# Optimization experiments

Measured on AMD Instinct MI355X. Metric: run time of the kernel, lower is better.

The kernel has to match this reference:

```python
import jax, jax.numpy as jnp
import numpy as np

WB = 8   # weight bit width (signed int8, power-of-two scale)
AB = 8   # activation bit width (uint8, power-of-two scale)
BB = 8   # bias bit width

# (name, c_in, c_out, kernel) for every QuantConv2d in order
_CFG = [("1", 3, 32, 3), ("2", 32, 16, 3), ("31", 16, 16, 1), ("32", 16, 32, 3),
        ("33", 32, 32, 1), ("34", 32, 64, 3), ("41", 64, 32, 1), ("42", 32, 64, 3),
        ("43", 64, 32, 1), ("44", 32, 64, 3), ("45", 64, 32, 1), ("46", 32, 64, 3)]
_POOL_AFTER = {"1", "2", "34"}  # MaxPool2d(2,2) follows these blocks


def _ste_round(x):
    # straight-through rounding (Brevitas-style fake quant)
    return x + jax.lax.stop_gradient(jnp.round(x) - x)


def _p2_scale(maxv, levels):
    # power-of-two (fixed point) per-tensor scale covering maxv with `levels` steps
    maxv = jnp.maximum(jax.lax.stop_gradient(maxv), 1e-8)
    return 2.0 ** jnp.ceil(jnp.log2(maxv / levels))


def quant_int(x, bw):
    # signed symmetric fixed-point fake quant (Int8WeightPerTensorFixedPoint style)
    n = 2.0 ** (bw - 1) - 1.0
    s = _p2_scale(jnp.max(jnp.abs(x)), n)
    return jnp.clip(_ste_round(x / s), -n - 1.0, n) * s


def quant_uint(x, bw):
    # unsigned fixed-point fake quant (Uint8ActPerTensorFixedPoint style)
    n = 2.0 ** bw - 1.0
    s = _p2_scale(jnp.max(x), n)
    return jnp.clip(_ste_round(x / s), 0.0, n) * s


def _conv(x, w, pad):
    return jax.lax.conv_general_dilated(
        x, w, window_strides=(1, 1), padding=[(pad, pad), (pad, pad)],
        dimension_numbers=("NCHW", "OIHW", "NCHW"))


def _maxpool2(x):
    return jax.lax.reduce_window(x, -jnp.inf, jax.lax.max,
                                 (1, 1, 2, 2), (1, 1, 2, 2), "VALID")


def _forward(x, p):
    # QuantIdentity on input (uint8 fixed point)
    x = quant_uint(x, AB)
    for n, ci, co, k in _CFG:
        pad = (k - 1) // 2
        y = _conv(x, quant_int(p["w" + n], WB), pad)               # quantized conv, no bias
        # BatchNorm2dToQuantScaleBias: per-channel affine with quantized scale/bias
        y = (y * quant_int(p["sg" + n], WB)[None, :, None, None]
             + quant_int(p["sb" + n], BB)[None, :, None, None])
        x = quant_uint(jax.nn.relu(y), AB)                          # QuantReLU
        if n in _POOL_AFTER:
            x = _maxpool2(x)
    # TruncAvgPool2d(28,28) over the remaining 28x28 map + RoundTo8bit requant
    x = quant_uint(jnp.mean(x, axis=(2, 3)), 8)                     # [B, 64]
    h = x @ quant_int(p["fw1"], WB).T + quant_int(p["fb1"], BB)     # linear51
    h = quant_uint(jax.nn.relu(h), AB)                              # relu5
    return h @ quant_int(p["fw2"], WB).T + quant_int(p["fb2"], BB)  # linear52


def setup_inputs() -> dict:
    key = jax.random.key(0)
    ks = iter(jax.random.split(key, 64))
    inp = {"x": jax.random.uniform(next(ks), (16, 3, 224, 224), jnp.float32)}
    for n, ci, co, k in _CFG:
        inp["w" + n] = jax.random.normal(next(ks), (co, ci, k, k), jnp.float32) * 0.1
        inp["sg" + n] = jax.random.uniform(next(ks), (co,), jnp.float32, 0.5, 1.5)
        inp["sb" + n] = jax.random.normal(next(ks), (co,), jnp.float32) * 0.1
    inp["fw1"] = jax.random.normal(next(ks), (16, 64), jnp.float32) * 0.1
    inp["fb1"] = jax.random.normal(next(ks), (16,), jnp.float32) * 0.1
    inp["fw2"] = jax.random.normal(next(ks), (10, 16), jnp.float32) * 0.1
    inp["fb2"] = jax.random.normal(next(ks), (10,), jnp.float32) * 0.1
    return inp


def reference(x, w1, sg1, sb1, w2, sg2, sb2, w31, sg31, sb31, w32, sg32, sb32,
              w33, sg33, sb33, w34, sg34, sb34, w41, sg41, sb41, w42, sg42, sb42,
              w43, sg43, sb43, w44, sg44, sb44, w45, sg45, sb45, w46, sg46, sb46,
              fw1, fb1, fw2, fb2):
    p = dict(locals())
    x = p.pop("x")
    return _forward(x, p)
```

## Files before the change

### kernel.cpp

```cpp
#include <hip/hip_runtime.h>
#include <math.h>

#define NL 12

typedef short v8s __attribute__((ext_vector_type(8)));
typedef float v4f __attribute__((ext_vector_type(4)));

struct PrepArgs {
  const float* in[40];
  void* out[40];
  int n[40];
  int mode[40];
  int tc[40];
  int ci[40], kk[40], kp[40], co[40];
};

__device__ inline float p2_scale_f(float maxv, float levels) {
  float r = __fdiv_rn(fmaxf(maxv, 1e-8f), levels);
  unsigned b = __float_as_uint(r);
  unsigned e = (b >> 23) & 0xffu;
  e += (b & 0x7fffffu) ? 1u : 0u;
  return __uint_as_float(e << 23);
}

__device__ inline float p2_inv(float s) {
  return __uint_as_float((254u << 23) - __float_as_uint(s));
}

__device__ inline float block_reduce_max256(float v) {
  __shared__ float sm[4];
  #pragma unroll
  for (int off = 32; off; off >>= 1) v = fmaxf(v, __shfl_down(v, off));
  if ((threadIdx.x & 63) == 0) sm[threadIdx.x >> 6] = v;
  __syncthreads();
  if (threadIdx.x == 0) v = fmaxf(fmaxf(sm[0], sm[1]), fmaxf(sm[2], sm[3]));
  return v;
}

__device__ inline void slot_max_update(float* slot, float v) {
  volatile unsigned int* su = (volatile unsigned int*)slot;
  unsigned int bits = __float_as_uint(v);
  if (bits > *su) atomicMax((unsigned int*)slot, bits);
}

__device__ inline short ibf16(float v) {
  return (short)(__float_as_uint(v) >> 16);
}

__global__ void prep_kernel(PrepArgs a, float* wslot,
                            const float* __restrict__ x, int nx, float* slot0) {
  if (blockIdx.x >= 40) {
    const float4* xv = (const float4*)x;
    const int nv = nx >> 2;
    float m0 = 0.f, m1 = 0.f, m2 = 0.f, m3 = 0.f;
    for (int i = (blockIdx.x - 40) * 256 + threadIdx.x; i < nv;
         i += (gridDim.x - 40) * 256) {
      float4 v = xv[i];
      m0 = fmaxf(m0, v.x); m1 = fmaxf(m1, v.y);
      m2 = fmaxf(m2, v.z); m3 = fmaxf(m3, v.w);
    }
    float m = fmaxf(fmaxf(m0, m1), fmaxf(m2, m3));
    float bm = block_reduce_max256(m);
    if (threadIdx.x == 0) slot_max_update(slot0, bm);
    return;
  }
  __shared__ float ssc;
  const int t = blockIdx.x;
  const float* in = a.in[t];
  const int n = a.n[t], mode = a.mode[t];
  float m = 0.f;
  if (mode >= 2) {
    const float4* in4 = (const float4*)in;
    const int n4 = n >> 2;
    for (int i = threadIdx.x; i < n4; i += 256) {
      float4 v = in4[i];
      m = fmaxf(m, fmaxf(fmaxf(fabsf(v.x), fabsf(v.y)),
                         fmaxf(fabsf(v.z), fabsf(v.w))));
    }
  } else {
    for (int i = threadIdx.x; i < n; i += 256) m = fmaxf(m, fabsf(in[i]));
  }
  float bm = block_reduce_max256(m);
  if (threadIdx.x == 0) {
    ssc = p2_scale_f(bm, 127.0f);
    if (mode >= 2) wslot[t] = ssc;
  }
  __syncthreads();
  const float s = ssc;
  if (mode == 3) {
    ushort* o = (ushort*)a.out[t];
    for (int i = threadIdx.x; i < 32 * 64; i += 256) {
      int co = i >> 6, k = i & 63;
      int khkw = k >> 2, ci = k & 3;
      ushort v = 0;
      if (khkw < 9 && ci < 3) {
        float q = rintf(__fdiv_rn(in[(co * 3 + ci) * 9 + khkw], s));
        q = fminf(fmaxf(q, -128.f), 127.f);
        v = (ushort)(__float_as_uint(q) >> 16);
      }
      o[i] = v;
    }
  } else if (mode == 2) {
    ushort* o = (ushort*)a.out[t];
    const int CI = a.ci[t], KK = a.kk[t], KP = a.kp[t], CO = a.co[t];
    const int KT = CI * KK;
    for (int i = threadIdx.x; i < CO * KP; i += 256) {
      int co = i / KP, k = i % KP;
      ushort v = 0;
      if (k < KT) {
        int khkw = k / CI, ci = k % CI;
        float q = rintf(__fdiv_rn(in[(co * CI + ci) * KK + khkw], s));
        q = fminf(fmaxf(q, -128.f), 127.f);
        v = (ushort)(__float_as_uint(q) >> 16);
      }
      o[i] = v;
    }
  } else {
    float* o = (float*)a.out[t];
    const int tc = a.tc[t];
    const int nw = (mode == 1) ? n / tc : 1;
    for (int i = threadIdx.x; i < n; i += 256) {
      float q = rintf(__fdiv_rn(in[i], s));
      q = fminf(fmaxf(q, -128.f), 127.f);
      float v = __fmul_rn(q, s);
      if (mode == 1) o[(i % nw) * tc + i / nw] = v;
      else o[i] = v;
    }
  }
}

__global__ void quantx_kernel(const float* __restrict__ x, ushort* __restrict__ xt,
                              const float* __restrict__ slot_in) {
  const float s = p2_scale_f(slot_in[0], 255.0f);
  const float inv = p2_inv(s);
  const int nh = blockIdx.x;
  const int w = threadIdx.x;
  if (w >= 224) return;
  const int n = nh / 224;
  const float* b0 = x + ((size_t)(n * 3 + 0) * 224 + (nh % 224)) * 224;
  const float* b1 = x + ((size_t)(n * 3 + 1) * 224 + (nh % 224)) * 224;
  const float* b2 = x + ((size_t)(n * 3 + 2) * 224 + (nh % 224)) * 224;
  ushort4 o;
  o.x = (ushort)ibf16(rintf(__fmul_rn(b0[w], inv)));
  o.y = (ushort)ibf16(rintf(__fmul_rn(b1[w], inv)));
  o.z = (ushort)ibf16(rintf(__fmul_rn(b2[w], inv)));
  o.w = 0;
  ((ushort4*)xt)[(size_t)nh * 224 + w] = o;
}


template <int CI, int H, int CO, bool POOL, int TOUT>
__global__ __launch_bounds__(256)
void conv_lds(const float* __restrict__ in, const short* __restrict__ wt,
              const float* __restrict__ sg, const float* __restrict__ sb,
              float* __restrict__ out, const float* __restrict__ slot_in,
              const float* __restrict__ wslotp, float* slot_out) {
  constexpr int W = H;
  constexpr int KT = 9 * CI;
  constexpr int SLABS = (KT + 31) / 32;
  constexpr int KP = SLABS * 32;
  constexpr int COT = CO / 16;
  constexpr int TIN = TOUT + 2;
  constexpr int NTL = (H + TOUT - 1) / TOUT;
  constexpr int PT = TOUT / 4;
  constexpr int NP = (PT * PT) / 4;
  constexpr int HO = POOL ? H / 2 : H;
  constexpr int WO = POOL ? W / 2 : W;
  constexpr int LG = (CI == 16) ? 2 : 3;
  constexpr int CH = CI / 4;

  __shared__ ushort lds[TIN * TIN * CI];

  const int lane = threadIdx.x & 63, widx = threadIdx.x >> 6;
  const int quad = lane >> 4, col = lane & 15;
  const float s_in = p2_scale_f(slot_in[0], 255.0f);
  const float inv = p2_inv(s_in);
  const float S = __fmul_rn(s_in, wslotp[0]);

  const int bt = blockIdx.x;
  const int n = bt / (NTL * NTL);
  const int rr = bt % (NTL * NTL);
  const int ty = rr / NTL, tx = rr % NTL;
  const int gh0 = ty * TOUT - 1, gw0 = tx * TOUT - 1;
  const float* ib = in + (size_t)n * H * W * CI;

  for (int i = threadIdx.x; i < TIN * TIN * CH; i += 256) {
    const int pix = i >> LG, cg = i & (CH - 1);
    const int hi = pix / TIN, wi = pix - hi * TIN;
    const int gh = gh0 + hi, gw = gw0 + wi;
    float4 f = {0.f, 0.f, 0.f, 0.f};
    if ((unsigned)gh < (unsigned)H && (unsigned)gw < (unsigned)W)
      f = *(const float4*)(ib + ((size_t)(gh * W + gw)) * CI + cg * 4);
    ushort4 c;
    c.x = (ushort)ibf16(rintf(__fmul_rn(f.x, inv)));
    c.y = (ushort)ibf16(rintf(__fmul_rn(f.y, inv)));
    c.z = (ushort)ibf16(rintf(__fmul_rn(f.z, inv)));
    c.w = (ushort)ibf16(rintf(__fmul_rn(f.w, inv)));
    ((ushort4*)lds)[i] = c;
  }
  __syncthreads();

  v4f acc[NP][COT];
  #pragma unroll
  for (int p = 0; p < NP; p++)
    #pragma unroll
    for (int c = 0; c < COT; c++) acc[p][c] = (v4f){0.f, 0.f, 0.f, 0.f};

  #pragma unroll
  for (int slab = 0; slab < SLABS; slab++) {
    const int kbase = slab * 32 + quad * 8;
    int tap = kbase / CI; tap = min(tap, 8);
    const int cib = kbase % CI;
    const int kh = tap / 3, kw = tap - kh * 3;
    v8s b[COT];
    #pragma unroll
    for (int c = 0; c < COT; c++)
      b[c] = *(const v8s*)(wt + (size_t)(c * 16 + col) * KP + kbase);
    #pragma unroll
    for (int p = 0; p < NP; p++) {
      const int q = widx * NP + p;
      const int plh = (q / PT) * 4, plw = (q % PT) * 4;
      const int hin = plh + (col >> 2) + kh, win = plw + (col & 3) + kw;
      v8s a = *(const v8s*)(lds + (hin * TIN + win) * CI + cib);
      #pragma unroll
      for (int c = 0; c < COT; c++)
        acc[p][c] = __builtin_amdgcn_mfma_f32_16x16x32_bf16(a, b[c], acc[p][c], 0, 0, 0);
    }
  }

  float zmax = 0.f;
  #pragma unroll
  for (int p = 0; p < NP; p++) {
    const int q = widx * NP + p;
    const int plh = (q / PT) * 4, plw = (q % PT) * 4;
    const int gho = ty * TOUT + plh, gwo = tx * TOUT + plw;
    #pragma unroll
    for (int c = 0; c < COT; c++) {
      const int cog = c * 16 + col;
      const float g = sg[cog], bb = sb[cog];
      float z[4];
      #pragma unroll
      for (int r2 = 0; r2 < 4; r2++) {
        float t = __fmul_rn(acc[p][c][r2], S);
        z[r2] = fmaxf(__fadd_rn(__fmul_rn(t, g), bb), 0.f);
      }
      if constexpr (POOL) {
        float h0 = fmaxf(z[0], z[1]), h1 = fmaxf(z[2], z[3]);
        float o0 = fmaxf(h0, __shfl_xor(h0, 16));
        float o1 = fmaxf(h1, __shfl_xor(h1, 16));
        const int oh = (gho >> 1) + (quad >> 1), ow = gwo >> 1;
        const bool v0 = (oh < HO) && (ow < WO), v1 = (oh < HO) && (ow + 1 < WO);
        zmax = fmaxf(zmax, fmaxf(v0 ? o0 : 0.f, v1 ? o1 : 0.f));
        if (!(quad & 1)) {
          float* op = out + ((size_t)((n * HO + oh) * WO + ow)) * CO + cog;
          if (v0) op[0] = o0;
          if (v1) op[CO] = o1;
        }
      } else {
        const int hh = gho + quad;
        #pragma unroll
        for (int r2 = 0; r2 < 4; r2++) {
          const int wwo = gwo + r2;
          if (hh < H && wwo < W) {
            out[(size_t)((n * H + hh) * W + wwo) * CO + cog] = z[r2];
            zmax = fmaxf(zmax, z[r2]);
          }
        }
      }
    }
  }
  float bm = block_reduce_max256(zmax);
  if (threadIdx.x == 0) slot_max_update(slot_out, bm);
}

__global__ __launch_bounds__(256)
void conv1_lds(const ushort* __restrict__ xt, const short* __restrict__ wt,
               const float* __restrict__ sg, const float* __restrict__ sb,
               float* __restrict__ out, const float* __restrict__ slot_in,
               const float* __restrict__ wslotp, float* slot_out) {
  constexpr int H = 224, W = 224, CO = 32, TOUT = 16, TIN = 18, NTL = 14;
  constexpr int HO = 112, WO = 112;
  __shared__ ushort lds[TIN * TIN * 4];

  const int lane = threadIdx.x & 63, widx = threadIdx.x >> 6;
  const int quad = lane >> 4, col = lane & 15;
  const float s_in = p2_scale_f(slot_in[0], 255.0f);
  const float S = __fmul_rn(s_in, wslotp[0]);

  const int bt = blockIdx.x;
  const int n = bt / (NTL * NTL);
  const int rr = bt % (NTL * NTL);
  const int ty = rr / NTL, tx = rr % NTL;
  const int gh0 = ty * TOUT - 1, gw0 = tx * TOUT - 1;
  const ushort* ib = xt + (size_t)n * H * W * 4;

  for (int i = threadIdx.x; i < TIN * TIN; i += 256) {
    const int hi = i / TIN, wi = i - hi * TIN;
    const int gh = gh0 + hi, gw = gw0 + wi;
    ushort4 c = {0, 0, 0, 0};
    if ((unsigned)gh < (unsigned)H && (unsigned)gw < (unsigned)W)
      c = *(const ushort4*)(ib + ((size_t)(gh * W + gw)) * 4);
    ((ushort4*)lds)[i] = c;
  }
  __syncthreads();

  const int plh = (widx >> 1) * 8, plwq = (widx & 1) * 8;
  v4f acc[4][2];
  #pragma unroll
  for (int p = 0; p < 4; p++) { acc[p][0] = (v4f){0,0,0,0}; acc[p][1] = acc[p][0]; }

  auto read4 = [&](int ph, int pw, int tap) -> ushort4 {
    const int hin = ph + (col >> 2) + tap / 3, win = pw + (col & 3) + tap % 3;
    return ((const ushort4*)lds)[hin * TIN + win];
  };

  #pragma unroll
  for (int slab = 0; slab < 2; slab++) {
    const int kbase = slab * 32 + quad * 8;
    int tA = slab * 8 + quad * 2; int tB = tA + 1;
    tA = min(tA, 8); tB = min(tB, 8);
    v8s b0 = *(const v8s*)(wt + (size_t)(col) * 64 + kbase);
    v8s b1 = *(const v8s*)(wt + (size_t)(16 + col) * 64 + kbase);
    #pragma unroll
    for (int p = 0; p < 4; p++) {
      const int ph = plh + (p >> 1) * 4, pw = plwq + (p & 1) * 4;
      ushort4 lo = read4(ph, pw, tA);
      ushort4 hi = read4(ph, pw, tB);
      v8s a;
      a[0] = (short)lo.x; a[1] = (short)lo.y; a[2] = (short)lo.z; a[3] = (short)lo.w;
      a[4] = (short)hi.x; a[5] = (short)hi.y; a[6] = (short)hi.z; a[7] = (short)hi.w;
      acc[p][0] = __builtin_amdgcn_mfma_f32_16x16x32_bf16(a, b0, acc[p][0], 0, 0, 0);
      acc[p][1] = __builtin_amdgcn_mfma_f32_16x16x32_bf16(a, b1, acc[p][1], 0, 0, 0);
    }
  }

  float zmax = 0.f;
  #pragma unroll
  for (int p = 0; p < 4; p++) {
    const int gho = ty * TOUT + plh + (p >> 1) * 4;
    const int gwo = tx * TOUT + plwq + (p & 1) * 4;
    #pragma unroll
    for (int c = 0; c < 2; c++) {
      const int cog = c * 16 + col;
      const float g = sg[cog], bb = sb[cog];
      float z[4];
      #pragma unroll
      for (int r2 = 0; r2 < 4; r2++) {
        float t = __fmul_rn(acc[p][c][r2], S);
        z[r2] = fmaxf(__fadd_rn(__fmul_rn(t, g), bb), 0.f);
      }
      float h0 = fmaxf(z[0], z[1]), h1 = fmaxf(z[2], z[3]);
      float o0 = fmaxf(h0, __shfl_xor(h0, 16));
      float o1 = fmaxf(h1, __shfl_xor(h1, 16));
      zmax = fmaxf(zmax, fmaxf(o0, o1));
      if (!(quad & 1)) {
        const int oh = (gho >> 1) + (quad >> 1), ow = gwo >> 1;
        float* op = out + ((size_t)((n * HO + oh) * WO + ow)) * CO + cog;
        op[0] = o0; op[CO] = o1;
      }
    }
  }
  float bm = block_reduce_max256(zmax);
  if (threadIdx.x == 0) slot_max_update(slot_out, bm);
}

template <int CI, int H, int CO, bool K3, bool POOL, int CSPLIT>
__global__ __launch_bounds__(256)
void conv_mfma(const float* __restrict__ in, const short* __restrict__ wt,
               const float* __restrict__ sg, const float* __restrict__ sb,
               float* __restrict__ out, const float* __restrict__ slot_in,
               const float* __restrict__ wslotp, float* slot_out) {
  constexpr int W = H;
  constexpr int KT = (K3 ? 9 : 1) * CI;
  constexpr int SLABS = (KT + 31) / 32;
  constexpr int KP = SLABS * 32;
  constexpr int COT = CO / (16 * CSPLIT);
  constexpr int HO = POOL ? H / 2 : H;
  constexpr int WO = POOL ? W / 2 : W;

  const int lane = threadIdx.x & 63, widx = threadIdx.x >> 6;
  const int quad = lane >> 4, col = lane & 15;
  const float s_in = p2_scale_f(slot_in[0], 255.0f);
  const float inv = p2_inv(s_in);
  const float S = __fmul_rn(s_in, wslotp[0]);
  const int wv = blockIdx.x * 4 + widx;
  const int mt = wv / CSPLIT, ct = wv % CSPLIT;

  int n, h, w, ph = 0, pw = 0;
  if constexpr (POOL) {
    constexpr int PB = (HO / 2) * (WO / 2);
    n = mt / PB; int r = mt % PB;
    ph = r / (WO / 2); pw = r % (WO / 2);
    h = 4 * ph + (col >> 2); w = 4 * pw + (col & 3);
  } else {
    int p = mt * 16 + col;
    n = p / (H * W); int r = p % (H * W);
    h = r / W; w = r % W;
  }
  const float* ibase = in + (size_t)n * H * W * CI;

  float4 fa[SLABS], fb[SLABS];
  bool vm[SLABS];
  #pragma unroll
  for (int slab = 0; slab < SLABS; slab++) {
    const int kbase = slab * 32 + quad * 8;
    const float* ap;
    if constexpr (K3) {
      const int khkw = min(kbase / CI, 8);
      const int cib = kbase % CI;
      const int kh = khkw / 3, kw = khkw - kh * 3;
      const int hh = h + kh - 1, ww = w + kw - 1;
      vm[slab] = (hh >= 0) && (hh < H) && (ww >= 0) && (ww < W);
      const int hc = min(max(hh, 0), H - 1), wc = min(max(ww, 0), W - 1);
      ap = ibase + (size_t)(hc * W + wc) * CI + cib;
    } else {
      vm[slab] = true;
      ap = ibase + (size_t)(h * W + w) * CI + (kbase % CI);
    }
    fa[slab] = ((const float4*)ap)[0];
    fb[slab] = ((const float4*)ap)[1];
  }

  v4f acc[COT];
  #pragma unroll
  for (int c = 0; c < COT; c++) acc[c] = (v4f){0.f, 0.f, 0.f, 0.f};

  #pragma unroll
  for (int slab = 0; slab < SLABS; slab++) {
    const int kbase = slab * 32 + quad * 8;
    float ff[8] = {fa[slab].x, fa[slab].y, fa[slab].z, fa[slab].w,
                   fb[slab].x, fb[slab].y, fb[slab].z, fb[slab].w};
    v8s a;
    #pragma unroll
    for (int j = 0; j < 8; j++) {
      float q = rintf(__fmul_rn(ff[j], inv));
      a[j] = vm[slab] ? ibf16(q) : (short)0;
    }
    #pragma unroll
    for (int c = 0; c < COT; c++) {
      v8s b = *(const v8s*)(wt + (size_t)((ct * COT + c) * 16 + col) * KP + kbase);
      acc[c] = __builtin_amdgcn_mfma_f32_16x16x32_bf16(a, b, acc[c], 0, 0, 0);
    }
  }

  float zmax = 0.f;
  #pragma unroll
  for (int c = 0; c < COT; c++) {
    const int cog = (ct * COT + c) * 16 + col;
    const float g = sg[cog], bb = sb[cog];
    float z[4];
    #pragma unroll
    for (int r2 = 0; r2 < 4; r2++) {
      float t = __fmul_rn(acc[c][r2], S);
      z[r2] = fmaxf(__fadd_rn(__fmul_rn(t, g), bb), 0.f);
    }
    if constexpr (POOL) {
      float h0 = fmaxf(z[0], z[1]), h1 = fmaxf(z[2], z[3]);
      float o0 = fmaxf(h0, __shfl_xor(h0, 16));
      float o1 = fmaxf(h1, __shfl_xor(h1, 16));
      zmax = fmaxf(zmax, fmaxf(o0, o1));
      if (!(quad & 1)) {
        int oh = 2 * ph + (quad >> 1), ow = 2 * pw;
        float* op = out + ((size_t)((n * HO + oh) * WO + ow)) * CO + cog;
        op[0] = o0; op[CO] = o1;
      }
    } else {
      const int pbase = mt * 16 + quad * 4;
      #pragma unroll
      for (int r2 = 0; r2 < 4; r2++) {
        out[(size_t)(pbase + r2) * CO + cog] = z[r2];
        zmax = fmaxf(zmax, z[r2]);
      }
    }
  }
  float bm = block_reduce_max256(zmax);
  if (threadIdx.x == 0) slot_max_update(slot_out, bm);
}

__global__ void avgpool_kernel(const float* __restrict__ in, float* __restrict__ out,
                               const float* __restrict__ slot_in, float* slot_out) {
  __shared__ float red[1024];
  const float s = p2_scale_f(slot_in[0], 255.0f);
  const float inv = p2_inv(s);
  const int nn = blockIdx.x, co = threadIdx.x & 63, part = threadIdx.x >> 6;
  const float* p = in + (size_t)nn * 784 * 64;
  float sum = 0.f;
  for (int i = part * 49; i < part * 49 + 49; i++)
    sum += __fmul_rn(rintf(__fmul_rn(p[i * 64 + co], inv)), s);
  red[threadIdx.x] = sum;
  __syncthreads();
  if (threadIdx.x < 64) {
    float tot = 0.f;
    #pragma unroll
    for (int k2 = 0; k2 < 16; k2++) tot += red[k2 * 64 + co];
    float m = __fdiv_rn(tot, 784.0f);
    out[nn * 64 + co] = m;
    slot_max_update(slot_out, m);
  }
}

__global__ void tail_kernel(const float* __restrict__ pooled,
                            const float* __restrict__ fw1, const float* __restrict__ fb1,
                            const float* __restrict__ fw2, const float* __restrict__ fb2,
                            const float* __restrict__ slot_in, float* __restrict__ out) {
  __shared__ float xq[1024];
  __shared__ float hq[256];
  __shared__ float s2s;
  const int t = threadIdx.x;
  const float s = p2_scale_f(slot_in[0], 255.0f);
  const float inv = p2_inv(s);
  for (int i = t; i < 1024; i += 256)
    xq[i] = __fmul_rn(rintf(__fmul_rn(pooled[i], inv)), s);
  __syncthreads();
  const int n = t >> 4, j = t & 15;
  float acc = 0.f;
  #pragma unroll 8
  for (int k = 0; k < 64; k++) acc += xq[n * 64 + k] * fw1[k * 16 + j];
  float z = fmaxf(__fadd_rn(acc, fb1[j]), 0.f);
  float bm = block_reduce_max256(z);
  if (t == 0) s2s = p2_scale_f(bm, 255.0f);
  __syncthreads();
  const float s2 = s2s, inv2 = p2_inv(s2);
  hq[t] = __fmul_rn(rintf(__fmul_rn(z, inv2)), s2);
  __syncthreads();
  if (t < 160) {
    const int n2 = t / 10, j2 = t % 10;
    float a2 = 0.f;
    #pragma unroll
    for (int k = 0; k < 16; k++) a2 += hq[n2 * 16 + k] * fw2[k * 10 + j2];
    out[t] = __fadd_rn(a2, fb2[j2]);
  }
}

extern "C" void kernel_launch(void* const* d_in, const int* in_sizes, int n_in,
                              void* d_out, int out_size, void* d_ws, size_t ws_size,
                              hipStream_t stream) {
  static const int h_ci[NL] = {3, 32, 16, 16, 32, 32, 64, 32, 64, 32, 64, 32};
  static const int h_co[NL] = {32, 16, 16, 32, 32, 64, 32, 64, 32, 64, 32, 64};
  static const int h_kk[NL] = {9, 9, 1, 9, 1, 9, 1, 9, 1, 9, 1, 9};
  static const int h_kp[NL] = {64, 288, 32, 160, 32, 288, 64, 288, 64, 288, 64, 288};

  float* ws = (float*)d_ws;
  float* slots = ws;
  float* wslot = ws + 16;
  size_t off = 32;

  short* wq[NL];
  for (int l = 0; l < NL; l++) {
    wq[l] = (short*)(ws + off);
    off += (size_t)(h_co[l] * h_kp[l] + 1) / 2;
  }
  float* sgq[NL]; float* sbq[NL];
  for (int l = 0; l < NL; l++) { sgq[l] = ws + off; off += 64; }
  for (int l = 0; l < NL; l++) { sbq[l] = ws + off; off += 64; }
  float* fw1q = ws + off; off += 1024;
  float* fb1q = ws + off; off += 16;
  float* fw2q = ws + off; off += 160;
  float* fb2q = ws + off; off += 16;
  off = (off + 1) & ~(size_t)1;
  ushort* XT = (ushort*)(ws + off); off += 1605632;
  float* A = ws + off; off += 6422528;
  float* B = ws + off; off += 1605632;
  float* P = ws + off; off += 1024;

  PrepArgs pa;
  for (int l = 0; l < NL; l++) {
    pa.in[l] = (const float*)d_in[1 + 3 * l]; pa.out[l] = (void*)wq[l];
    pa.n[l] = h_co[l] * h_ci[l] * h_kk[l];
    pa.mode[l] = (l == 0) ? 3 : 2; pa.tc[l] = 0;
    pa.ci[l] = h_ci[l]; pa.kk[l] = h_kk[l]; pa.kp[l] = h_kp[l]; pa.co[l] = h_co[l];
    pa.in[12 + l] = (const float*)d_in[2 + 3 * l]; pa.out[12 + l] = (void*)sgq[l];
    pa.n[12 + l] = h_co[l]; pa.mode[12 + l] = 0; pa.tc[12 + l] = 0;
    pa.ci[12 + l] = pa.kk[12 + l] = pa.kp[12 + l] = pa.co[12 + l] = 0;
    pa.in[24 + l] = (const float*)d_in[3 + 3 * l]; pa.out[24 + l] = (void*)sbq[l];
    pa.n[24 + l] = h_co[l]; pa.mode[24 + l] = 0; pa.tc[24 + l] = 0;
    pa.ci[24 + l] = pa.kk[24 + l] = pa.kp[24 + l] = pa.co[24 + l] = 0;
  }
  pa.in[36] = (const float*)d_in[37]; pa.out[36] = (void*)fw1q;
  pa.n[36] = 1024; pa.mode[36] = 1; pa.tc[36] = 16;
  pa.ci[36] = pa.kk[36] = pa.kp[36] = pa.co[36] = 0;
  pa.in[37] = (const float*)d_in[38]; pa.out[37] = (void*)fb1q;
  pa.n[37] = 16; pa.mode[37] = 0; pa.tc[37] = 0;
  pa.ci[37] = pa.kk[37] = pa.kp[37] = pa.co[37] = 0;
  pa.in[38] = (const float*)d_in[39]; pa.out[38] = (void*)fw2q;
  pa.n[38] = 160; pa.mode[38] = 1; pa.tc[38] = 10;
  pa.ci[38] = pa.kk[38] = pa.kp[38] = pa.co[38] = 0;
  pa.in[39] = (const float*)d_in[40]; pa.out[39] = (void*)fb2q;
  pa.n[39] = 10; pa.mode[39] = 0; pa.tc[39] = 0;
  pa.ci[39] = pa.kk[39] = pa.kp[39] = pa.co[39] = 0;

  const float* x = (const float*)d_in[0];
  const int nx = 16 * 3 * 224 * 224;

  hipMemsetAsync(slots, 0, 16 * sizeof(float), stream);
  prep_kernel<<<40 + 294, 256, 0, stream>>>(pa, wslot, x, nx, slots + 0);
  quantx_kernel<<<16 * 224, 256, 0, stream>>>(x, XT, slots + 0);

  conv1_lds<<<16 * 14 * 14, 256, 0, stream>>>(XT, wq[0], sgq[0], sbq[0], A,
                                              slots + 0, wslot + 0, slots + 1);
  conv_lds<32, 112, 16, true, 16><<<16 * 49, 256, 0, stream>>>(
      A, wq[1], sgq[1], sbq[1], B, slots + 1, wslot + 1, slots + 2);
  conv_mfma<16, 56, 16, false, false, 1><<<784, 256, 0, stream>>>(
      B, wq[2], sgq[2], sbq[2], A, slots + 2, wslot + 2, slots + 3);
  conv_lds<16, 56, 32, false, 16><<<16 * 16, 256, 0, stream>>>(
      A, wq[3], sgq[3], sbq[3], B, slots + 3, wslot + 3, slots + 4);
  conv_mfma<32, 56, 32, false, false, 2><<<1568, 256, 0, stream>>>(
      B, wq[4], sgq[4], sbq[4], A, slots + 4, wslot + 4, slots + 5);
  conv_lds<32, 56, 64, true, 16><<<16 * 16, 256, 0, stream>>>(
      A, wq[5], sgq[5], sbq[5], B, slots + 5, wslot + 5, slots + 6);
  conv_mfma<64, 28, 32, false, false, 2><<<392, 256, 0, stream>>>(
      B, wq[6], sgq[6], sbq[6], A, slots + 6, wslot + 6, slots + 7);
  conv_lds<32, 28, 64, false, 8><<<16 * 16, 256, 0, stream>>>(
      A, wq[7], sgq[7], sbq[7], B, slots + 7, wslot + 7, slots + 8);
  conv_mfma<64, 28, 32, false, false, 2><<<392, 256, 0, stream>>>(
      B, wq[8], sgq[8], sbq[8], A, slots + 8, wslot + 8, slots + 9);
  conv_lds<32, 28, 64, false, 8><<<16 * 16, 256, 0, stream>>>(
      A, wq[9], sgq[9], sbq[9], B, slots + 9, wslot + 9, slots + 10);
  conv_mfma<64, 28, 32, false, false, 2><<<392, 256, 0, stream>>>(
      B, wq[10], sgq[10], sbq[10], A, slots + 10, wslot + 10, slots + 11);
  conv_lds<32, 28, 64, false, 8><<<16 * 16, 256, 0, stream>>>(
      A, wq[11], sgq[11], sbq[11], B, slots + 11, wslot + 11, slots + 12);

  avgpool_kernel<<<16, 1024, 0, stream>>>(B, P, slots + 12, slots + 13);
  tail_kernel<<<1, 256, 0, stream>>>(P, fw1q, fb1q, fw2q, fb2q, slots + 13,
                                     (float*)d_out);
}
```

Before: 330.1 us.

## Fuse 28x28 conv stages and avgpool into one cooperative mega-kernel

Replaces the six 28x28 conv launches and the avgpool kernel with a single cooperative kernel of 16 blocks (one per image) of 1024 threads. Each block keeps its image's quantized activations in a swizzled LDS tile and uses grid-wide syncs to exchange the per-tensor max scale between layers. This removes launch overhead and global round-trips for the requantized codes. The cost is that only 16 CUs do the work, so compute parallelism drops sharply, and grid.sync adds latency per layer.

```diff
diff --git a/kernel.cpp b/kernel.cpp
--- a/kernel.cpp
+++ b/kernel.cpp
@@ -1,4 +1,5 @@
 #include <hip/hip_runtime.h>
+#include <hip/hip_cooperative_groups.h>
 #include <math.h>
 
 #define NL 12
@@ -147,7 +148,6 @@
   o.w = 0;
   ((ushort4*)xt)[(size_t)nh * 224 + w] = o;
 }
-
 
 template <int CI, int H, int CO, bool POOL, int TOUT>
 __global__ __launch_bounds__(256)
@@ -477,25 +477,189 @@
   if (threadIdx.x == 0) slot_max_update(slot_out, bm);
 }
 
-__global__ void avgpool_kernel(const float* __restrict__ in, float* __restrict__ out,
-                               const float* __restrict__ slot_in, float* slot_out) {
+
+struct MegaArgs {
+  const float* in;
+  float* scratch;
+  const short* w[6];
+  const float* sg[6];
+  const float* sb[6];
+  const float* wslot;
+  float* slots;
+  float* P;
+};
+
+__device__ inline int cswz(int pix, int ch) {
+  return pix * 64 + (ch ^ ((pix & 7) << 3));
+}
+
+__device__ inline float block_reduce_max1024(float v, float* red) {
+  #pragma unroll
+  for (int off = 32; off; off >>= 1) v = fmaxf(v, __shfl_down(v, off));
+  if ((threadIdx.x & 63) == 0) red[threadIdx.x >> 6] = v;
+  __syncthreads();
+  float m = v;
+  if (threadIdx.x == 0) {
+    m = red[0];
+    #pragma unroll
+    for (int i = 1; i < 16; i++) m = fmaxf(m, red[i]);
+  }
+  __syncthreads();
+  return m;
+}
+
+template <int CH4>
+__device__ inline void mega_requant(const float* __restrict__ src0, float inv,
+                                    ushort* codes) {
+  const float4* src = (const float4*)src0;
+  for (int i = threadIdx.x; i < 784 * CH4; i += 1024) {
+    const int p = i / CH4, cg4 = i - p * CH4;
+    const int h = p / 28, w = p - h * 28;
+    float4 f = src[i];
+    ushort4 c;
+    c.x = (ushort)ibf16(rintf(__fmul_rn(f.x, inv)));
+    c.y = (ushort)ibf16(rintf(__fmul_rn(f.y, inv)));
+    c.z = (ushort)ibf16(rintf(__fmul_rn(f.z, inv)));
+    c.w = (ushort)ibf16(rintf(__fmul_rn(f.w, inv)));
+    *(ushort4*)(codes + cswz((1 + h) * 30 + 1 + w, cg4 * 4)) = c;
+  }
+}
+
+__device__ inline void mega_k1(const MegaArgs& a, int L, const ushort* codes,
+                               float* red) {
+  const int tid = threadIdx.x, lane = tid & 63;
+  const int widx = tid >> 6, quad = lane >> 4, col = lane & 15;
+  const float s_in = p2_scale_f(a.slots[6 + L], 255.0f);
+  const float S = __fmul_rn(s_in, a.wslot[6 + L]);
+  const short* wt = a.w[L];
+  const float* sg = a.sg[L]; const float* sb = a.sb[L];
+  float* raw = a.scratch + (size_t)blockIdx.x * 784 * 32;
+  float zmax = 0.f;
+  for (int p = widx; p < 49; p += 16) {
+    const int plh = (p / 7) * 4, plw = (p % 7) * 4;
+    const int pix = (1 + plh + (col >> 2)) * 30 + 1 + plw + (col & 3);
+    v4f acc[2];
+    acc[0] = (v4f){0.f, 0.f, 0.f, 0.f}; acc[1] = acc[0];
+    #pragma unroll
+    for (int slab = 0; slab < 2; slab++) {
+      const int kbase = slab * 32 + quad * 8;
+      v8s av = *(const v8s*)(codes + cswz(pix, kbase));
+      #pragma unroll
+      for (int c = 0; c < 2; c++) {
+        v8s b = *(const v8s*)(wt + (size_t)(c * 16 + col) * 64 + kbase);
+        acc[c] = __builtin_amdgcn_mfma_f32_16x16x32_bf16(av, b, acc[c], 0, 0, 0);
+      }
+    }
+    #pragma unroll
+    for (int c = 0; c < 2; c++) {
+      const int cog = c * 16 + col;
+      const float g = sg[cog], bb = sb[cog];
+      #pragma unroll
+      for (int r2 = 0; r2 < 4; r2++) {
+        float t = __fmul_rn(acc[c][r2], S);
+        float z = fmaxf(__fadd_rn(__fmul_rn(t, g), bb), 0.f);
+        raw[(size_t)((plh + quad) * 28 + plw + r2) * 32 + cog] = z;
+        zmax = fmaxf(zmax, z);
+      }
+    }
+  }
+  float bm = block_reduce_max1024(zmax, red);
+  if (tid == 0) slot_max_update(a.slots + 7 + L, bm);
+}
+
+__device__ inline void mega_k3(const MegaArgs& a, int L, const ushort* codes,
+                               float* red) {
+  const int tid = threadIdx.x, lane = tid & 63;
+  const int widx = tid >> 6, quad = lane >> 4, col = lane & 15;
+  const float s_in = p2_scale_f(a.slots[6 + L], 255.0f);
+  const float S = __fmul_rn(s_in, a.wslot[6 + L]);
+  const short* wt = a.w[L];
+  const float* sg = a.sg[L]; const float* sb = a.sb[L];
+  float* raw = a.scratch + (size_t)blockIdx.x * 784 * 64;
+  float zmax = 0.f;
+  for (int p = widx; p < 49; p += 16) {
+    const int plh = (p / 7) * 4, plw = (p % 7) * 4;
+    v4f acc[4];
+    acc[0] = (v4f){0.f, 0.f, 0.f, 0.f};
+    acc[1] = acc[0]; acc[2] = acc[0]; acc[3] = acc[0];
+    const int cib = quad * 8;
+    #pragma unroll
+    for (int slab = 0; slab < 9; slab++) {
+      const int kh = slab / 3, kw = slab - kh * 3;
+      const int pix = (plh + (col >> 2) + kh) * 30 + plw + (col & 3) + kw;
+      v8s av = *(const v8s*)(codes + cswz(pix, cib));
+      const int kbase = slab * 32 + cib;
+      #pragma unroll
+      for (int c = 0; c < 4; c++) {
+        v8s b = *(const v8s*)(wt + (size_t)(c * 16 + col) * 288 + kbase);
+        acc[c] = __builtin_amdgcn_mfma_f32_16x16x32_bf16(av, b, acc[c], 0, 0, 0);
+      }
+    }
+    #pragma unroll
+    for (int c = 0; c < 4; c++) {
+      const int cog = c * 16 + col;
+      const float g = sg[cog], bb = sb[cog];
+      #pragma unroll
+      for (int r2 = 0; r2 < 4; r2++) {
+        float t = __fmul_rn(acc[c][r2], S);
+        float z = fmaxf(__fadd_rn(__fmul_rn(t, g), bb), 0.f);
+        raw[(size_t)((plh + quad) * 28 + plw + r2) * 64 + cog] = z;
+        zmax = fmaxf(zmax, z);
+      }
+    }
+  }
+  float bm = block_reduce_max1024(zmax, red);
+  if (tid == 0) slot_max_update(a.slots + 7 + L, bm);
+}
+
+__global__ __launch_bounds__(1024)
+void mega28(MegaArgs a) {
+  cooperative_groups::grid_group grid = cooperative_groups::this_grid();
+  __shared__ ushort codes[30 * 30 * 64];
   __shared__ float red[1024];
-  const float s = p2_scale_f(slot_in[0], 255.0f);
-  const float inv = p2_inv(s);
-  const int nn = blockIdx.x, co = threadIdx.x & 63, part = threadIdx.x >> 6;
-  const float* p = in + (size_t)nn * 784 * 64;
-  float sum = 0.f;
-  for (int i = part * 49; i < part * 49 + 49; i++)
-    sum += __fmul_rn(rintf(__fmul_rn(p[i * 64 + co], inv)), s);
-  red[threadIdx.x] = sum;
-  __syncthreads();
-  if (threadIdx.x < 64) {
-    float tot = 0.f;
-    #pragma unroll
-    for (int k2 = 0; k2 < 16; k2++) tot += red[k2 * 64 + co];
-    float m = __fdiv_rn(tot, 784.0f);
-    out[nn * 64 + co] = m;
-    slot_max_update(slot_out, m);
+  const int tid = threadIdx.x;
+
+  for (int i = tid; i < 30 * 30 * 64 / 4; i += 1024)
+    ((ushort4*)codes)[i] = (ushort4){0, 0, 0, 0};
+  __syncthreads();
+
+  mega_requant<16>(a.in + (size_t)blockIdx.x * 784 * 64,
+                   p2_inv(p2_scale_f(a.slots[6], 255.0f)), codes);
+  __syncthreads();
+
+  #pragma unroll
+  for (int l = 0; l < 3; l++) {
+    const int L1 = 2 * l, L3 = 2 * l + 1;
+    mega_k1(a, L1, codes, red);
+    grid.sync();
+    mega_requant<8>(a.scratch + (size_t)blockIdx.x * 784 * 32,
+                    p2_inv(p2_scale_f(a.slots[7 + L1], 255.0f)), codes);
+    __syncthreads();
+    mega_k3(a, L3, codes, red);
+    grid.sync();
+    mega_requant<16>(a.scratch + (size_t)blockIdx.x * 784 * 64,
+                     p2_inv(p2_scale_f(a.slots[7 + L3], 255.0f)), codes);
+    __syncthreads();
+  }
+
+  {
+    const float s = p2_scale_f(a.slots[12], 255.0f);
+    const int co = tid & 63, part = tid >> 6;
+    float sum = 0.f;
+    for (int i = part * 49; i < part * 49 + 49; i++) {
+      const int h = i / 28, w = i - h * 28;
+      sum += __uint_as_float((unsigned)codes[cswz((1 + h) * 30 + 1 + w, co)] << 16);
+    }
+    red[tid] = sum;
+    __syncthreads();
+    if (tid < 64) {
+      float tot = 0.f;
+      #pragma unroll
+      for (int k2 = 0; k2 < 16; k2++) tot += red[k2 * 64 + co];
+      float m = __fdiv_rn(__fmul_rn(tot, s), 784.0f);
+      a.P[blockIdx.x * 64 + co] = m;
+      slot_max_update(a.slots + 13, m);
+    }
   }
 }
 
@@ -608,20 +772,17 @@
       B, wq[4], sgq[4], sbq[4], A, slots + 4, wslot + 4, slots + 5);
   conv_lds<32, 56, 64, true, 16><<<16 * 16, 256, 0, stream>>>(
       A, wq[5], sgq[5], sbq[5], B, slots + 5, wslot + 5, slots + 6);
-  conv_mfma<64, 28, 32, false, false, 2><<<392, 256, 0, stream>>>(
-      B, wq[6], sgq[6], sbq[6], A, slots + 6, wslot + 6, slots + 7);
-  conv_lds<32, 28, 64, false, 8><<<16 * 16, 256, 0, stream>>>(
-      A, wq[7], sgq[7], sbq[7], B, slots + 7, wslot + 7, slots + 8);
-  conv_mfma<64, 28, 32, false, false, 2><<<392, 256, 0, stream>>>(
-      B, wq[8], sgq[8], sbq[8], A, slots + 8, wslot + 8, slots + 9);
-  conv_lds<32, 28, 64, false, 8><<<16 * 16, 256, 0, stream>>>(
-      A, wq[9], sgq[9], sbq[9], B, slots + 9, wslot + 9, slots + 10);
-  conv_mfma<64, 28, 32, false, false, 2><<<392, 256, 0, stream>>>(
-      B, wq[10], sgq[10], sbq[10], A, slots + 10, wslot + 10, slots + 11);
-  conv_lds<32, 28, 64, false, 8><<<16 * 16, 256, 0, stream>>>(
-      A, wq[11], sgq[11], sbq[11], B, slots + 11, wslot + 11, slots + 12);
-
-  avgpool_kernel<<<16, 1024, 0, stream>>>(B, P, slots + 12, slots + 13);
+
+  MegaArgs ma;
+  ma.in = B; ma.scratch = A;
+  for (int l = 0; l < 6; l++) {
+    ma.w[l] = wq[6 + l]; ma.sg[l] = sgq[6 + l]; ma.sb[l] = sbq[6 + l];
+  }
+  ma.wslot = wslot; ma.slots = slots; ma.P = P;
+  void* margs[] = {&ma};
+  hipLaunchCooperativeKernel((const void*)mega28, dim3(16), dim3(1024),
+                             margs, 0, stream);
+
   tail_kernel<<<1, 256, 0, stream>>>(P, fw1q, fb1q, fw2q, fb2q, slots + 13,
                                      (float*)d_out);
 }
```

New measurement: 495.4 us. +50.1%, slower.

## Fuse input quantization into conv1 and XOR-swizzle LDS layout for CI=32

Applied to the files above, without the earlier changes.

Removes the separate quantx kernel and its bf16 NHWC staging buffer; conv1 now reads the NCHW float input directly, quantizes it, and writes the codes into shared memory. This drops one launch and a global write plus read of the transposed input, at the cost of scalar strided loads from three channel planes. Separately, conv_lds with 32 input channels now XOR-swizzles the channel offset by pixel index in LDS to reduce bank conflicts on the MFMA operand reads.

```diff
diff --git a/kernel.cpp b/kernel.cpp
--- a/kernel.cpp
+++ b/kernel.cpp
@@ -127,25 +127,6 @@
       else o[i] = v;
     }
   }
-}
-
-__global__ void quantx_kernel(const float* __restrict__ x, ushort* __restrict__ xt,
-                              const float* __restrict__ slot_in) {
-  const float s = p2_scale_f(slot_in[0], 255.0f);
-  const float inv = p2_inv(s);
-  const int nh = blockIdx.x;
-  const int w = threadIdx.x;
-  if (w >= 224) return;
-  const int n = nh / 224;
-  const float* b0 = x + ((size_t)(n * 3 + 0) * 224 + (nh % 224)) * 224;
-  const float* b1 = x + ((size_t)(n * 3 + 1) * 224 + (nh % 224)) * 224;
-  const float* b2 = x + ((size_t)(n * 3 + 2) * 224 + (nh % 224)) * 224;
-  ushort4 o;
-  o.x = (ushort)ibf16(rintf(__fmul_rn(b0[w], inv)));
-  o.y = (ushort)ibf16(rintf(__fmul_rn(b1[w], inv)));
-  o.z = (ushort)ibf16(rintf(__fmul_rn(b2[w], inv)));
-  o.w = 0;
-  ((ushort4*)xt)[(size_t)nh * 224 + w] = o;
 }
 
 
@@ -171,6 +152,11 @@
 
   __shared__ ushort lds[TIN * TIN * CI];
 
+  auto lidx = [](int pix, int cs) -> int {
+    if constexpr (CI == 32) return pix * CI + (cs ^ ((pix & 3) << 3));
+    else return pix * CI + cs;
+  };
+
   const int lane = threadIdx.x & 63, widx = threadIdx.x >> 6;
   const int quad = lane >> 4, col = lane & 15;
   const float s_in = p2_scale_f(slot_in[0], 255.0f);
@@ -196,7 +182,7 @@
     c.y = (ushort)ibf16(rintf(__fmul_rn(f.y, inv)));
     c.z = (ushort)ibf16(rintf(__fmul_rn(f.z, inv)));
     c.w = (ushort)ibf16(rintf(__fmul_rn(f.w, inv)));
-    ((ushort4*)lds)[i] = c;
+    *(ushort4*)(lds + lidx(pix, cg * 4)) = c;
   }
   __syncthreads();
 
@@ -221,7 +207,7 @@
       const int q = widx * NP + p;
       const int plh = (q / PT) * 4, plw = (q % PT) * 4;
       const int hin = plh + (col >> 2) + kh, win = plw + (col & 3) + kw;
-      v8s a = *(const v8s*)(lds + (hin * TIN + win) * CI + cib);
+      v8s a = *(const v8s*)(lds + lidx(hin * TIN + win, cib));
       #pragma unroll
       for (int c = 0; c < COT; c++)
         acc[p][c] = __builtin_amdgcn_mfma_f32_16x16x32_bf16(a, b[c], acc[p][c], 0, 0, 0);
@@ -274,7 +260,7 @@
 }
 
 __global__ __launch_bounds__(256)
-void conv1_lds(const ushort* __restrict__ xt, const short* __restrict__ wt,
+void conv1_lds(const float* __restrict__ x, const short* __restrict__ wt,
                const float* __restrict__ sg, const float* __restrict__ sb,
                float* __restrict__ out, const float* __restrict__ slot_in,
                const float* __restrict__ wslotp, float* slot_out) {
@@ -285,6 +271,7 @@
   const int lane = threadIdx.x & 63, widx = threadIdx.x >> 6;
   const int quad = lane >> 4, col = lane & 15;
   const float s_in = p2_scale_f(slot_in[0], 255.0f);
+  const float inv = p2_inv(s_in);
   const float S = __fmul_rn(s_in, wslotp[0]);
 
   const int bt = blockIdx.x;
@@ -292,16 +279,18 @@
   const int rr = bt % (NTL * NTL);
   const int ty = rr / NTL, tx = rr % NTL;
   const int gh0 = ty * TOUT - 1, gw0 = tx * TOUT - 1;
-  const ushort* ib = xt + (size_t)n * H * W * 4;
-
-  for (int i = threadIdx.x; i < TIN * TIN; i += 256) {
-    const int hi = i / TIN, wi = i - hi * TIN;
+  const float* xb = x + (size_t)n * 3 * H * W;
+
+  for (int i = threadIdx.x; i < 3 * TIN * TIN; i += 256) {
+    const int c = i / (TIN * TIN), pix = i - c * TIN * TIN;
+    const int hi = pix / TIN, wi = pix - hi * TIN;
     const int gh = gh0 + hi, gw = gw0 + wi;
-    ushort4 c = {0, 0, 0, 0};
+    ushort code = 0;
     if ((unsigned)gh < (unsigned)H && (unsigned)gw < (unsigned)W)
-      c = *(const ushort4*)(ib + ((size_t)(gh * W + gw)) * 4);
-    ((ushort4*)lds)[i] = c;
-  }
+      code = (ushort)ibf16(rintf(__fmul_rn(xb[(size_t)c * H * W + gh * W + gw], inv)));
+    lds[pix * 4 + c] = code;
+  }
+  for (int i = threadIdx.x; i < TIN * TIN; i += 256) lds[i * 4 + 3] = 0;
   __syncthreads();
 
   const int plh = (widx >> 1) * 8, plwq = (widx & 1) * 8;
@@ -557,8 +546,6 @@
   float* fb1q = ws + off; off += 16;
   float* fw2q = ws + off; off += 160;
   float* fb2q = ws + off; off += 16;
-  off = (off + 1) & ~(size_t)1;
-  ushort* XT = (ushort*)(ws + off); off += 1605632;
   float* A = ws + off; off += 6422528;
   float* B = ws + off; off += 1605632;
   float* P = ws + off; off += 1024;
@@ -594,9 +581,8 @@
 
   hipMemsetAsync(slots, 0, 16 * sizeof(float), stream);
   prep_kernel<<<40 + 294, 256, 0, stream>>>(pa, wslot, x, nx, slots + 0);
-  quantx_kernel<<<16 * 224, 256, 0, stream>>>(x, XT, slots + 0);
-
-  conv1_lds<<<16 * 14 * 14, 256, 0, stream>>>(XT, wq[0], sgq[0], sbq[0], A,
+
+  conv1_lds<<<16 * 14 * 14, 256, 0, stream>>>(x, wq[0], sgq[0], sbq[0], A,
                                               slots + 0, wslot + 0, slots + 1);
   conv_lds<32, 112, 16, true, 16><<<16 * 49, 256, 0, stream>>>(
       A, wq[1], sgq[1], sbq[1], B, slots + 1, wslot + 1, slots + 2);
```

New measurement: 330.6 us. Within noise of the previous version (+0.2%).
